# Optimization experiments

Measured on AMD Instinct MI355X. Metric: run time of the kernel, lower is better.

## Reference

```python
import jax, jax.numpy as jnp
import numpy as np

B, S, D = 4, 1024, 1024   # batch, seq_len, d_model (isize=hsize=osize)
H, AD = 16, 64            # num_head, attn_dim = hsize // num_head
K_REL = 16                # k_rel_pos (bidirectional: 2*K+1 = 33 embeddings)
EPS = 1e-8                # SparseNormer eps (ieps_default)


def setup_inputs() -> dict:
    key = jax.random.key(0)
    ks = jax.random.split(key, 5)
    scale = 0.02
    return {
        "iQ": jax.random.normal(ks[0], (B, S, D), jnp.float32),
        "Wa": jax.random.normal(ks[1], (3 * D, D), jnp.float32) * scale,   # adaptor weight
        "ba": jnp.zeros((3 * D,), jnp.float32),                            # adaptor bias
        "rel_emb": jax.random.normal(ks[2], (2 * K_REL + 1, AD), jnp.float32) * scale,
        "sn_bias": jnp.zeros((1,), jnp.float32),                           # SparseNormer bias
        "Wo": jax.random.normal(ks[3], (D, D), jnp.float32) * scale,       # outer weight
        "bo": jnp.zeros((D,), jnp.float32),                                # outer bias
    }


def reference(iQ, Wa, ba, rel_emb, sn_bias, Wo, bo):
    b, s, _ = iQ.shape
    # fused QKV projection: [B,S,3*H*AD] -> q,k,v each [B,H,S,AD]
    qkv = (iQ @ Wa.T + ba).reshape(b, s, 3, H, AD)
    q = qkv[:, :, 0].transpose(0, 2, 1, 3)
    k = qkv[:, :, 1].transpose(0, 2, 1, 3)
    v = qkv[:, :, 2].transpose(0, 2, 1, 3)

    # content scores [B,H,S,S]
    scores = jnp.einsum('bhqd,bhkd->bhqk', q, k)

    # relative-position term: rel_pos[i,j] = clip(j-i, -K, K) + K
    pos = jnp.arange(s)
    rp = jnp.clip(pos[None, :] - pos[:, None], -K_REL, K_REL) + K_REL  # [S,S] int
    r = rel_emb[rp]                                                     # [S,S,AD]
    scores = scores + jnp.einsum('bhqd,qkd->bhqk', q, r)

    scores = scores / jnp.sqrt(jnp.asarray(AD, scores.dtype))

    # SparseNormer: relu(x + b)^2 / (sum + eps)
    t = jax.nn.relu(scores + sn_bias)
    t = t * t
    attn = t / (t.sum(-1, keepdims=True) + EPS)

    ctx = jnp.einsum('bhqk,bhkd->bhqd', attn, v)          # [B,H,S,AD]
    ctx = ctx.transpose(0, 2, 1, 3).reshape(b, s, H * AD)  # [B,S,hsize]
    return ctx @ Wo.T + bo
```

## Files before the change

### kernel.cpp

```cpp
#include <hip/hip_runtime.h>
#include <hip/hip_bf16.h>
#include <stdint.h>

typedef unsigned short u16;
typedef unsigned int   u32;
typedef __attribute__((ext_vector_type(8))) __bf16 bf16x8;
typedef __attribute__((ext_vector_type(4))) float  f32x4;
typedef __attribute__((ext_vector_type(2))) u32    u32x2;

#define B_  4
#define S_  1024
#define D_  1024
#define H_  16
#define AD_ 64

#if defined(__has_builtin)
#if __has_builtin(__builtin_amdgcn_cvt_pk_bf16_f32)
#define HAVE_CVT_PK 1
#endif
#if __has_builtin(__builtin_amdgcn_global_load_lds)
#define HAVE_GLL 1
#endif
#endif

#ifdef HAVE_CVT_PK
typedef __attribute__((ext_vector_type(2))) __bf16 bf16x2;
__device__ __forceinline__ u32 pack2(float a, float b) {
    bf16x2 r = __builtin_amdgcn_cvt_pk_bf16_f32(a, b);
    return __builtin_bit_cast(u32, r);
}
__device__ __forceinline__ u16 f2bf(float f) {
    return (u16)pack2(f, f);
}
#else
__device__ __forceinline__ u16 f2bf(float f) {
    u32 u = __float_as_uint(f);
    u32 r = u + 0x7fffu + ((u >> 16) & 1u);
    return (u16)(r >> 16);
}
__device__ __forceinline__ u32 pack2(float a, float b) {
    return (u32)f2bf(a) | ((u32)f2bf(b) << 16);
}
#endif

typedef __attribute__((address_space(1))) const u32 gas_u32;
typedef __attribute__((address_space(3))) u32 las_u32;
__device__ __forceinline__ void gll16(const void* g, void* l) {
#ifdef HAVE_GLL
    __builtin_amdgcn_global_load_lds((gas_u32*)g, (las_u32*)l, 16, 0, 0);
#else
    int lane = threadIdx.x & 63;
    *(uint4*)((u16*)l + lane * 8) = *(const uint4*)g;
#endif
}

__global__ __launch_bounds__(256) void conv_bf16(
    const float* __restrict__ a, const float* __restrict__ b,
    const float* __restrict__ c,
    u16* __restrict__ ao, u16* __restrict__ bo, u16* __restrict__ co,
    int na, int nb)
{
    int gid = blockIdx.x * 256 + threadIdx.x;
    int base = gid * 8;
    const float* src; u16* dst; int off;
    if (base < na)           { src = a; dst = ao; off = base; }
    else if (base < na + nb) { src = b; dst = bo; off = base - na; }
    else                     { src = c; dst = co; off = base - na - nb; }
    float4 v0 = *(const float4*)(src + off);
    float4 v1 = *(const float4*)(src + off + 4);
    u32 pk[4] = {pack2(v0.x, v0.y), pack2(v0.z, v0.w),
                 pack2(v1.x, v1.y), pack2(v1.z, v1.w)};
    *(uint4*)(dst + off) = *(uint4*)pk;
}

__global__ __launch_bounds__(256) void qkv_gemm(
    const u16* __restrict__ A, const u16* __restrict__ W,
    const float* __restrict__ bias,
    u16* __restrict__ qb, u16* __restrict__ kb, u16* __restrict__ vb)
{
    __shared__ u16 As[128 * 64];
    __shared__ u16 Bs[128 * 64];

    const int tid  = threadIdx.x;
    const int lane = tid & 63, w = tid >> 6;
    const int quad = lane >> 4, ln = lane & 15;
    const int wrow = (w >> 1) * 64, wcol = (w & 1) * 64;
    const int row0 = blockIdx.y * 128, col0 = blockIdx.x * 128;

    const int ri = lane >> 3, ci = lane & 7;
    const int scol = (ci ^ ri) << 3;

    f32x4 acc[4][4];
#pragma unroll
    for (int i = 0; i < 4; i++)
#pragma unroll
        for (int j = 0; j < 4; j++) acc[i][j] = (f32x4){0.f, 0.f, 0.f, 0.f};

    for (int kb_i = 0; kb_i < 16; ++kb_i) {
        const int k0 = kb_i * 64;
#pragma unroll
        for (int c = 0; c < 4; ++c) {
            int r0 = c * 32 + w * 8;
            int gr = r0 + ri;
            gll16(A + (size_t)(row0 + gr) * D_ + k0 + scol, &As[r0 * 64]);
            gll16(W + (size_t)(col0 + gr) * D_ + k0 + scol, &Bs[r0 * 64]);
        }
        __syncthreads();
#pragma unroll
        for (int ks = 0; ks < 2; ++ks) {
            bf16x8 af[4], bfr[4];
#pragma unroll
            for (int mt = 0; mt < 4; ++mt) {
                int r = wrow + mt * 16 + ln;
                af[mt] = *(bf16x8*)&As[r * 64 + (((ks * 4 + quad) ^ (r & 7)) << 3)];
            }
#pragma unroll
            for (int nt = 0; nt < 4; ++nt) {
                int r = wcol + nt * 16 + ln;
                bfr[nt] = *(bf16x8*)&Bs[r * 64 + (((ks * 4 + quad) ^ (r & 7)) << 3)];
            }
#pragma unroll
            for (int mt = 0; mt < 4; ++mt)
#pragma unroll
                for (int nt = 0; nt < 4; ++nt)
                    acc[mt][nt] = __builtin_amdgcn_mfma_f32_16x16x32_bf16(
                        af[mt], bfr[nt], acc[mt][nt], 0, 0, 0);
        }
        __syncthreads();
    }

    const int which = col0 >> 10;
#pragma unroll
    for (int mt = 0; mt < 4; ++mt) {
#pragma unroll
        for (int nt = 0; nt < 4; ++nt) {
            int n = col0 + wcol + nt * 16 + ln;
            float bv = bias[n];
            int h = (n >> 6) & 15, d = n & 63;
            if (which == 2) {
                int m0 = row0 + wrow + mt * 16 + quad * 4;
                int b = m0 >> 10, s0 = m0 & 1023;
                u32x2 pk;
                pk.x = pack2(acc[mt][nt][0] + bv, acc[mt][nt][1] + bv);
                pk.y = pack2(acc[mt][nt][2] + bv, acc[mt][nt][3] + bv);
                *(u32x2*)&vb[((size_t)((b * 16 + h) * 64 + d)) * 1024 + s0] = pk;
            } else {
#pragma unroll
                for (int reg = 0; reg < 4; ++reg) {
                    int m = row0 + wrow + mt * 16 + quad * 4 + reg;
                    int b = m >> 10, s = m & 1023;
                    float v = acc[mt][nt][reg] + bv;
                    if (which == 0)
                        qb[((size_t)((b * 16 + h) * 1024 + s)) * 64 + d] = f2bf(v * 0.125f);
                    else
                        kb[((size_t)((b * 16 + h) * 1024 + s)) * 64 + d] = f2bf(v);
                }
            }
        }
    }
}

__global__ __launch_bounds__(256) void attn_kernel(
    const u16* __restrict__ qb, const u16* __restrict__ kb,
    const u16* __restrict__ vb, const float* __restrict__ rel,
    const float* __restrict__ snb_p, u16* __restrict__ ctx)
{
    __shared__ u16 q_s[64 * 64];
    __shared__ u16 k_s[64 * 64];
    __shared__ u16 v_s[64 * 64];
    __shared__ u16 t_s[64 * 64];
    __shared__ float qr[33 * 64];

    u16* rel_s = t_s;

    const int tid  = threadIdx.x;
    const int lane = tid & 63, w = tid >> 6;
    const int quad = lane >> 4, ln = lane & 15;
    const int strip = w * 16;
    const int bh = blockIdx.x >> 4, qt = blockIdx.x & 15;
    const int i0 = qt * 64;
    const float snb = snb_p[0];

    const u16* qplane = qb + ((size_t)bh * 1024 + i0) * 64;
    const u16* kplane = kb + (size_t)bh * 1024 * 64;
    const u16* vplane = vb + (size_t)bh * 64 * 1024;

    const int ri = lane >> 3, ci = lane & 7;
    const int scol = (ci ^ ri) << 3;

#pragma unroll
    for (int c = 0; c < 2; ++c) {
        int r0 = w * 16 + c * 8;
        int gr = r0 + ri;
        gll16(qplane + (size_t)gr * 64 + scol, &q_s[r0 * 64]);
    }
    for (int idx = tid; idx < 384; idx += 256) {
        int p = idx >> 3, c = idx & 7;
        u32 pk[4];
        if (p < 33) {
            const float* sp = rel + p * 64 + c * 8;
            float4 r0 = *(const float4*)sp;
            float4 r1 = *(const float4*)(sp + 4);
            pk[0] = pack2(r0.x, r0.y); pk[1] = pack2(r0.z, r0.w);
            pk[2] = pack2(r1.x, r1.y); pk[3] = pack2(r1.z, r1.w);
        } else { pk[0] = pk[1] = pk[2] = pk[3] = 0; }
        *(uint4*)&rel_s[p * 64 + ((c ^ (p & 7)) << 3)] = *(uint4*)pk;
    }
    __syncthreads();

    {
        f32x4 qacc[3];
#pragma unroll
        for (int nt = 0; nt < 3; ++nt) qacc[nt] = (f32x4){0.f, 0.f, 0.f, 0.f};
#pragma unroll
        for (int ks = 0; ks < 2; ++ks) {
            int rq = strip + ln;
            bf16x8 aq = *(bf16x8*)&q_s[rq * 64 + (((ks * 4 + quad) ^ (rq & 7)) << 3)];
#pragma unroll
            for (int nt = 0; nt < 3; ++nt) {
                int rp = nt * 16 + ln;
                bf16x8 bp = *(bf16x8*)&rel_s[rp * 64 + (((ks * 4 + quad) ^ (rp & 7)) << 3)];
                qacc[nt] = __builtin_amdgcn_mfma_f32_16x16x32_bf16(aq, bp, qacc[nt], 0, 0, 0);
            }
        }
#pragma unroll
        for (int nt = 0; nt < 3; ++nt) {
            int p = nt * 16 + ln;
            if (p < 33) {
#pragma unroll
                for (int reg = 0; reg < 4; ++reg)
                    qr[p * 64 + strip + quad * 4 + reg] = qacc[nt][reg];
            }
        }
    }
    __syncthreads();

    const int iloc = strip + ln;
    const float cL = qr[iloc] + snb;
    const float cR = qr[32 * 64 + iloc] + snb;

    bf16x8 bq[2];
#pragma unroll
    for (int ks = 0; ks < 2; ++ks)
        bq[ks] = *(bf16x8*)&q_s[iloc * 64 + (((ks * 4 + quad) ^ (iloc & 7)) << 3)];

    float Lsum = 0.f;
    f32x4 o_acc[4];
#pragma unroll
    for (int nt = 0; nt < 4; ++nt) o_acc[nt] = (f32x4){0.f, 0.f, 0.f, 0.f};

    for (int jt = 0; jt < 16; ++jt) {
        const int j0 = jt * 64;
        __syncthreads();
#pragma unroll
        for (int c = 0; c < 2; ++c) {
            int r0 = w * 16 + c * 8;
            int gr = r0 + ri;
            gll16(kplane + (size_t)(j0 + gr) * 64 + scol, &k_s[r0 * 64]);
            gll16(vplane + (size_t)gr * 1024 + j0 + scol, &v_s[r0 * 64]);
        }
        __syncthreads();

        f32x4 sacc[4];
#pragma unroll
        for (int mj = 0; mj < 4; ++mj) sacc[mj] = (f32x4){0.f, 0.f, 0.f, 0.f};
#pragma unroll
        for (int ks = 0; ks < 2; ++ks) {
#pragma unroll
            for (int mj = 0; mj < 4; ++mj) {
                int rk = mj * 16 + ln;
                bf16x8 ak = *(bf16x8*)&k_s[rk * 64 + (((ks * 4 + quad) ^ (rk & 7)) << 3)];
                sacc[mj] = __builtin_amdgcn_mfma_f32_16x16x32_bf16(ak, bq[ks], sacc[mj], 0, 0, 0);
            }
        }

        const int d0 = j0 - i0;
        if (d0 <= -128 || d0 >= 128) {
            const float c = (d0 < 0) ? cL : cR;
#pragma unroll
            for (int mj = 0; mj < 4; ++mj) {
                float tv[4];
#pragma unroll
                for (int reg = 0; reg < 4; ++reg) {
                    float t = fmaxf(sacc[mj][reg] + c, 0.f);
                    t = t * t;
                    Lsum += t;
                    tv[reg] = t;
                }
                u32x2 pk;
                pk.x = pack2(tv[0], tv[1]);
                pk.y = pack2(tv[2], tv[3]);
                int jl = mj * 16 + quad * 4;
                int chunk = (jl >> 3) ^ (iloc & 7);
                *(u32x2*)&t_s[iloc * 64 + (chunk << 3) + (quad & 1) * 4] = pk;
            }
        } else {
#pragma unroll
            for (int mj = 0; mj < 4; ++mj) {
                int jbase = j0 + mj * 16 + quad * 4;
                float tv[4];
#pragma unroll
                for (int reg = 0; reg < 4; ++reg) {
                    int dlt = jbase + reg - (i0 + iloc);
                    int p = min(max(dlt, -16), 16) + 16;
                    float t = fmaxf(sacc[mj][reg] + qr[p * 64 + iloc] + snb, 0.f);
                    t = t * t;
                    Lsum += t;
                    tv[reg] = t;
                }
                u32x2 pk;
                pk.x = pack2(tv[0], tv[1]);
                pk.y = pack2(tv[2], tv[3]);
                int jl = mj * 16 + quad * 4;
                int chunk = (jl >> 3) ^ (iloc & 7);
                *(u32x2*)&t_s[iloc * 64 + (chunk << 3) + (quad & 1) * 4] = pk;
            }
        }

#pragma unroll
        for (int ks = 0; ks < 2; ++ks) {
            bf16x8 at = *(bf16x8*)&t_s[iloc * 64 + (((ks * 4 + quad) ^ (iloc & 7)) << 3)];
#pragma unroll
            for (int nt = 0; nt < 4; ++nt) {
                int rv = nt * 16 + ln;
                bf16x8 bv = *(bf16x8*)&v_s[rv * 64 + (((ks * 4 + quad) ^ (rv & 7)) << 3)];
                o_acc[nt] = __builtin_amdgcn_mfma_f32_16x16x32_bf16(at, bv, o_acc[nt], 0, 0, 0);
            }
        }
    }

    Lsum += __shfl_xor(Lsum, 16);
    Lsum += __shfl_xor(Lsum, 32);
    float Linv = 1.f / (Lsum + 1e-8f);

    const int b = bh >> 4, h = bh & 15;
#pragma unroll
    for (int reg = 0; reg < 4; ++reg) {
        int ig = i0 + strip + quad * 4 + reg;
        float li = __shfl(Linv, quad * 4 + reg);
#pragma unroll
        for (int nt = 0; nt < 4; ++nt) {
            int dg = nt * 16 + ln;
            ctx[((size_t)(b * 1024 + ig)) * 1024 + h * 64 + dg] =
                f2bf(o_acc[nt][reg] * li);
        }
    }
}

__global__ __launch_bounds__(256) void out_gemm(
    const u16* __restrict__ A, const u16* __restrict__ W,
    const float* __restrict__ bias, float* __restrict__ out)
{
    __shared__ u16 As[128 * 64];
    __shared__ u16 Bs[128 * 64];

    const int tid  = threadIdx.x;
    const int lane = tid & 63, w = tid >> 6;
    const int quad = lane >> 4, ln = lane & 15;
    const int wrow = (w >> 1) * 64, wcol = (w & 1) * 64;
    const int row0 = blockIdx.y * 128, col0 = blockIdx.x * 128;

    const int ri = lane >> 3, ci = lane & 7;
    const int scol = (ci ^ ri) << 3;

    f32x4 acc[4][4];
#pragma unroll
    for (int i = 0; i < 4; i++)
#pragma unroll
        for (int j = 0; j < 4; j++) acc[i][j] = (f32x4){0.f, 0.f, 0.f, 0.f};

    for (int kb_i = 0; kb_i < 16; ++kb_i) {
        const int k0 = kb_i * 64;
#pragma unroll
        for (int c = 0; c < 4; ++c) {
            int r0 = c * 32 + w * 8;
            int gr = r0 + ri;
            gll16(A + (size_t)(row0 + gr) * D_ + k0 + scol, &As[r0 * 64]);
            gll16(W + (size_t)(col0 + gr) * D_ + k0 + scol, &Bs[r0 * 64]);
        }
        __syncthreads();
#pragma unroll
        for (int ks = 0; ks < 2; ++ks) {
            bf16x8 af[4], bfr[4];
#pragma unroll
            for (int mt = 0; mt < 4; ++mt) {
                int r = wrow + mt * 16 + ln;
                af[mt] = *(bf16x8*)&As[r * 64 + (((ks * 4 + quad) ^ (r & 7)) << 3)];
            }
#pragma unroll
            for (int nt = 0; nt < 4; ++nt) {
                int r = wcol + nt * 16 + ln;
                bfr[nt] = *(bf16x8*)&Bs[r * 64 + (((ks * 4 + quad) ^ (r & 7)) << 3)];
            }
#pragma unroll
            for (int mt = 0; mt < 4; ++mt)
#pragma unroll
                for (int nt = 0; nt < 4; ++nt)
                    acc[mt][nt] = __builtin_amdgcn_mfma_f32_16x16x32_bf16(
                        af[mt], bfr[nt], acc[mt][nt], 0, 0, 0);
        }
        __syncthreads();
    }
#pragma unroll
    for (int mt = 0; mt < 4; ++mt) {
#pragma unroll
        for (int nt = 0; nt < 4; ++nt) {
            int n = col0 + wcol + nt * 16 + ln;
            float bv = bias[n];
#pragma unroll
            for (int reg = 0; reg < 4; ++reg) {
                int m = row0 + wrow + mt * 16 + quad * 4 + reg;
                out[(size_t)m * D_ + n] = acc[mt][nt][reg] + bv;
            }
        }
    }
}

extern "C" void kernel_launch(void* const* d_in, const int* in_sizes, int n_in,
                              void* d_out, int out_size, void* d_ws, size_t ws_size,
                              hipStream_t stream)
{
    const float* iQ  = (const float*)d_in[0];
    const float* Wa  = (const float*)d_in[1];
    const float* ba  = (const float*)d_in[2];
    const float* rel = (const float*)d_in[3];
    const float* snb = (const float*)d_in[4];
    const float* Wo  = (const float*)d_in[5];
    const float* bo  = (const float*)d_in[6];
    float* out = (float*)d_out;

    const size_t NQ = (size_t)B_ * S_ * D_;
    const size_t NWA = (size_t)3 * D_ * D_;
    const size_t NWO = (size_t)D_ * D_;
    const size_t PLANE = (size_t)B_ * H_ * S_ * AD_;

    u16* iQbf = (u16*)d_ws;
    u16* Wabf = iQbf + NQ;
    u16* Wobf = Wabf + NWA;
    u16* qbuf = Wobf + NWO;
    u16* kbuf = qbuf + PLANE;
    u16* vbuf = kbuf + PLANE;
    u16* ctx  = iQbf;

    conv_bf16<<<4096, 256, 0, stream>>>(iQ, Wa, Wo, iQbf, Wabf, Wobf,
                                        (int)NQ, (int)NWA);
    qkv_gemm<<<dim3(24, 32), 256, 0, stream>>>(iQbf, Wabf, ba, qbuf, kbuf, vbuf);
    attn_kernel<<<dim3(1024), 256, 0, stream>>>(qbuf, kbuf, vbuf, rel, snb, ctx);
    out_gemm<<<dim3(8, 32), 256, 0, stream>>>(ctx, Wobf, bo, out);
}
```

Before: 196.7 us.

## Fuse all stages into one persistent cooperative kernel with grid syncs

Replaces the four separate launches (bf16 conversion, QKV GEMM, attention, output GEMM) with a single persistent cooperative kernel. Blocks loop over tiles and separate the stages with grid-wide syncs, which removes launch gaps and inter-kernel drains. The attention stage also double-buffers the K/V tiles so the next tile is prefetched during compute, and the output GEMM uses 128x64 tiles so more blocks can share the work. The costs are grid.sync overhead, a grid capped by occupancy that may leave some stages underfilled, and a fallback to the multi-kernel path if the cooperative launch fails.

```diff
diff --git a/kernel.cpp b/kernel.cpp
--- a/kernel.cpp
+++ b/kernel.cpp
@@ -1,6 +1,9 @@
 #include <hip/hip_runtime.h>
+#include <hip/hip_cooperative_groups.h>
 #include <hip/hip_bf16.h>
 #include <stdint.h>
+
+namespace cg = cooperative_groups;
 
 typedef unsigned short u16;
 typedef unsigned int   u32;
@@ -29,9 +32,7 @@
     bf16x2 r = __builtin_amdgcn_cvt_pk_bf16_f32(a, b);
     return __builtin_bit_cast(u32, r);
 }
-__device__ __forceinline__ u16 f2bf(float f) {
-    return (u16)pack2(f, f);
-}
+__device__ __forceinline__ u16 f2bf(float f) { return (u16)pack2(f, f); }
 #else
 __device__ __forceinline__ u16 f2bf(float f) {
     u32 u = __float_as_uint(f);
@@ -52,6 +53,374 @@
     int lane = threadIdx.x & 63;
     *(uint4*)((u16*)l + lane * 8) = *(const uint4*)g;
 #endif
+}
+
+#define SMEM_BYTES 49408
+
+__global__ void __launch_bounds__(256, 3) fused_pipeline(
+    const float* __restrict__ iQ, const float* __restrict__ Wa,
+    const float* __restrict__ ba, const float* __restrict__ rel,
+    const float* __restrict__ snb_p, const float* __restrict__ Wo,
+    const float* __restrict__ bo, float* __restrict__ out,
+    u16* iQbf, u16* Wabf, u16* Wobf, u16* qbuf, u16* kbuf, u16* vbuf)
+{
+    __shared__ __align__(16) char smem[SMEM_BYTES];
+    cg::grid_group grid = cg::this_grid();
+    const int nblk = gridDim.x;
+
+    const int tid  = threadIdx.x;
+    const int lane = tid & 63, w = tid >> 6;
+    const int quad = lane >> 4, ln = lane & 15;
+    const int ri = lane >> 3, ci = lane & 7;
+    const int scol = (ci ^ ri) << 3;
+
+    {
+        const int NQ = B_ * S_ * D_;
+        const int NWA = 3 * D_ * D_;
+        const int NT = NQ + NWA + D_ * D_;
+        const int stride = nblk * 256 * 8;
+        for (int base = (blockIdx.x * 256 + tid) * 8; base < NT; base += stride) {
+            const float* src; u16* dst; int off;
+            if (base < NQ)            { src = iQ; dst = iQbf; off = base; }
+            else if (base < NQ + NWA) { src = Wa; dst = Wabf; off = base - NQ; }
+            else                      { src = Wo; dst = Wobf; off = base - NQ - NWA; }
+            float4 v0 = *(const float4*)(src + off);
+            float4 v1 = *(const float4*)(src + off + 4);
+            u32 pk[4] = {pack2(v0.x, v0.y), pack2(v0.z, v0.w),
+                         pack2(v1.x, v1.y), pack2(v1.z, v1.w)};
+            *(uint4*)(dst + off) = *(uint4*)pk;
+        }
+    }
+    __threadfence();
+    grid.sync();
+
+    {
+        u16* As = (u16*)smem;
+        u16* Bs = (u16*)(smem + 16384);
+        const int wrow = (w >> 1) * 64, wcol = (w & 1) * 64;
+
+        for (int t = blockIdx.x; t < 768; t += nblk) {
+            const int row0 = (t / 24) * 128, col0 = (t % 24) * 128;
+
+            f32x4 acc[4][4];
+#pragma unroll
+            for (int i = 0; i < 4; i++)
+#pragma unroll
+                for (int j = 0; j < 4; j++) acc[i][j] = (f32x4){0.f, 0.f, 0.f, 0.f};
+
+            for (int kb_i = 0; kb_i < 16; ++kb_i) {
+                const int k0 = kb_i * 64;
+#pragma unroll
+                for (int c = 0; c < 4; ++c) {
+                    int r0 = c * 32 + w * 8;
+                    int gr = r0 + ri;
+                    gll16(iQbf + (size_t)(row0 + gr) * D_ + k0 + scol, &As[r0 * 64]);
+                    gll16(Wabf + (size_t)(col0 + gr) * D_ + k0 + scol, &Bs[r0 * 64]);
+                }
+                __syncthreads();
+#pragma unroll
+                for (int ks = 0; ks < 2; ++ks) {
+                    bf16x8 af[4], bfr[4];
+#pragma unroll
+                    for (int mt = 0; mt < 4; ++mt) {
+                        int r = wrow + mt * 16 + ln;
+                        af[mt] = *(bf16x8*)&As[r * 64 + (((ks * 4 + quad) ^ (r & 7)) << 3)];
+                    }
+#pragma unroll
+                    for (int nt = 0; nt < 4; ++nt) {
+                        int r = wcol + nt * 16 + ln;
+                        bfr[nt] = *(bf16x8*)&Bs[r * 64 + (((ks * 4 + quad) ^ (r & 7)) << 3)];
+                    }
+#pragma unroll
+                    for (int mt = 0; mt < 4; ++mt)
+#pragma unroll
+                        for (int nt = 0; nt < 4; ++nt)
+                            acc[mt][nt] = __builtin_amdgcn_mfma_f32_16x16x32_bf16(
+                                af[mt], bfr[nt], acc[mt][nt], 0, 0, 0);
+                }
+                __syncthreads();
+            }
+
+            const int which = col0 >> 10;
+#pragma unroll
+            for (int mt = 0; mt < 4; ++mt) {
+#pragma unroll
+                for (int nt = 0; nt < 4; ++nt) {
+                    int n = col0 + wcol + nt * 16 + ln;
+                    float bv = ba[n];
+                    int h = (n >> 6) & 15, d = n & 63;
+                    if (which == 2) {
+                        int m0 = row0 + wrow + mt * 16 + quad * 4;
+                        int b = m0 >> 10, s0 = m0 & 1023;
+                        u32x2 pk;
+                        pk.x = pack2(acc[mt][nt][0] + bv, acc[mt][nt][1] + bv);
+                        pk.y = pack2(acc[mt][nt][2] + bv, acc[mt][nt][3] + bv);
+                        *(u32x2*)&vbuf[((size_t)((b * 16 + h) * 64 + d)) * 1024 + s0] = pk;
+                    } else {
+#pragma unroll
+                        for (int reg = 0; reg < 4; ++reg) {
+                            int m = row0 + wrow + mt * 16 + quad * 4 + reg;
+                            int b = m >> 10, s = m & 1023;
+                            float v = acc[mt][nt][reg] + bv;
+                            if (which == 0)
+                                qbuf[((size_t)((b * 16 + h) * 1024 + s)) * 64 + d] = f2bf(v * 0.125f);
+                            else
+                                kbuf[((size_t)((b * 16 + h) * 1024 + s)) * 64 + d] = f2bf(v);
+                        }
+                    }
+                }
+            }
+        }
+    }
+    __threadfence();
+    grid.sync();
+
+    {
+        u16* q_s = (u16*)smem;
+        u16* k0b = (u16*)(smem + 8192);
+        u16* k1b = (u16*)(smem + 16384);
+        u16* v0b = (u16*)(smem + 24576);
+        u16* v1b = (u16*)(smem + 32768);
+        float* qr = (float*)(smem + 40960);
+        u16* t_s = q_s;
+        u16* rel_s = v1b;
+
+        u16* ctx = iQbf;
+        const float snb = snb_p[0];
+        const int strip = w * 16;
+
+        for (int t = blockIdx.x; t < 1024; t += nblk) {
+            const int bh = t >> 4, qt = t & 15;
+            const int i0 = qt * 64;
+            const u16* qplane = qbuf + ((size_t)bh * 1024 + i0) * 64;
+            const u16* kplane = kbuf + (size_t)bh * 1024 * 64;
+            const u16* vplane = vbuf + (size_t)bh * 64 * 1024;
+
+#pragma unroll
+            for (int c = 0; c < 2; ++c) {
+                int r0 = strip + c * 8;
+                gll16(qplane + (size_t)(r0 + ri) * 64 + scol, &q_s[r0 * 64]);
+            }
+            for (int idx = tid; idx < 384; idx += 256) {
+                int p = idx >> 3, c = idx & 7;
+                u32 pk[4];
+                if (p < 33) {
+                    const float* sp = rel + p * 64 + c * 8;
+                    float4 r0 = *(const float4*)sp;
+                    float4 r1 = *(const float4*)(sp + 4);
+                    pk[0] = pack2(r0.x, r0.y); pk[1] = pack2(r0.z, r0.w);
+                    pk[2] = pack2(r1.x, r1.y); pk[3] = pack2(r1.z, r1.w);
+                } else { pk[0] = pk[1] = pk[2] = pk[3] = 0; }
+                *(uint4*)&rel_s[p * 64 + ((c ^ (p & 7)) << 3)] = *(uint4*)pk;
+            }
+            __syncthreads();
+
+            const int iloc = strip + ln;
+            bf16x8 bq[2];
+#pragma unroll
+            for (int ks = 0; ks < 2; ++ks)
+                bq[ks] = *(bf16x8*)&q_s[iloc * 64 + (((ks * 4 + quad) ^ (iloc & 7)) << 3)];
+
+            {
+                f32x4 qacc[3];
+#pragma unroll
+                for (int nt = 0; nt < 3; ++nt) qacc[nt] = (f32x4){0.f, 0.f, 0.f, 0.f};
+#pragma unroll
+                for (int ks = 0; ks < 2; ++ks) {
+#pragma unroll
+                    for (int nt = 0; nt < 3; ++nt) {
+                        int rp = nt * 16 + ln;
+                        bf16x8 bp = *(bf16x8*)&rel_s[rp * 64 + (((ks * 4 + quad) ^ (rp & 7)) << 3)];
+                        qacc[nt] = __builtin_amdgcn_mfma_f32_16x16x32_bf16(bq[ks], bp, qacc[nt], 0, 0, 0);
+                    }
+                }
+#pragma unroll
+                for (int nt = 0; nt < 3; ++nt) {
+                    int p = nt * 16 + ln;
+                    if (p < 33) {
+#pragma unroll
+                        for (int reg = 0; reg < 4; ++reg)
+                            qr[p * 64 + strip + quad * 4 + reg] = qacc[nt][reg];
+                    }
+                }
+            }
+#pragma unroll
+            for (int c = 0; c < 2; ++c) {
+                int r0 = strip + c * 8;
+                gll16(kplane + (size_t)(r0 + ri) * 64 + scol, &k0b[r0 * 64]);
+                gll16(vplane + (size_t)(r0 + ri) * 1024 + scol, &v0b[r0 * 64]);
+            }
+            __syncthreads();
+
+            const float cL = qr[iloc] + snb;
+            const float cR = qr[32 * 64 + iloc] + snb;
+
+            float Lsum = 0.f;
+            f32x4 o_acc[4];
+#pragma unroll
+            for (int nt = 0; nt < 4; ++nt) o_acc[nt] = (f32x4){0.f, 0.f, 0.f, 0.f};
+
+            for (int jt = 0; jt < 16; ++jt) {
+                const int j0 = jt * 64;
+                u16* kc = (jt & 1) ? k1b : k0b;
+                u16* vc = (jt & 1) ? v1b : v0b;
+                if (jt < 15) {
+                    u16* kn = (jt & 1) ? k0b : k1b;
+                    u16* vn = (jt & 1) ? v0b : v1b;
+#pragma unroll
+                    for (int c = 0; c < 2; ++c) {
+                        int r0 = strip + c * 8;
+                        gll16(kplane + (size_t)(j0 + 64 + r0 + ri) * 64 + scol, &kn[r0 * 64]);
+                        gll16(vplane + (size_t)(r0 + ri) * 1024 + (j0 + 64) + scol, &vn[r0 * 64]);
+                    }
+                }
+
+                f32x4 sacc[4];
+#pragma unroll
+                for (int mj = 0; mj < 4; ++mj) sacc[mj] = (f32x4){0.f, 0.f, 0.f, 0.f};
+#pragma unroll
+                for (int ks = 0; ks < 2; ++ks) {
+#pragma unroll
+                    for (int mj = 0; mj < 4; ++mj) {
+                        int rk = mj * 16 + ln;
+                        bf16x8 ak = *(bf16x8*)&kc[rk * 64 + (((ks * 4 + quad) ^ (rk & 7)) << 3)];
+                        sacc[mj] = __builtin_amdgcn_mfma_f32_16x16x32_bf16(ak, bq[ks], sacc[mj], 0, 0, 0);
+                    }
+                }
+
+                const int ib = i0 + strip;
+#pragma unroll
+                for (int mj = 0; mj < 4; ++mj) {
+                    const int jg0 = j0 + mj * 16;
+                    const int diff = jg0 - ib;
+                    float tv[4];
+                    if (diff >= 32 || diff <= -32) {
+                        const float c = (diff < 0) ? cL : cR;
+#pragma unroll
+                        for (int reg = 0; reg < 4; ++reg) {
+                            float tt = fmaxf(sacc[mj][reg] + c, 0.f);
+                            tt = tt * tt;
+                            Lsum += tt;
+                            tv[reg] = tt;
+                        }
+                    } else {
+#pragma unroll
+                        for (int reg = 0; reg < 4; ++reg) {
+                            int dlt = jg0 + quad * 4 + reg - (ib + ln);
+                            int p = min(max(dlt, -16), 16) + 16;
+                            float tt = fmaxf(sacc[mj][reg] + qr[p * 64 + iloc] + snb, 0.f);
+                            tt = tt * tt;
+                            Lsum += tt;
+                            tv[reg] = tt;
+                        }
+                    }
+                    u32x2 pk;
+                    pk.x = pack2(tv[0], tv[1]);
+                    pk.y = pack2(tv[2], tv[3]);
+                    int chunk = (2 * mj + (quad >> 1)) ^ (iloc & 7);
+                    *(u32x2*)&t_s[iloc * 64 + (chunk << 3) + (quad & 1) * 4] = pk;
+                }
+
+#pragma unroll
+                for (int ks = 0; ks < 2; ++ks) {
+                    bf16x8 at = *(bf16x8*)&t_s[iloc * 64 + (((ks * 4 + quad) ^ (iloc & 7)) << 3)];
+#pragma unroll
+                    for (int nt = 0; nt < 4; ++nt) {
+                        int rv = nt * 16 + ln;
+                        bf16x8 bv = *(bf16x8*)&vc[rv * 64 + (((ks * 4 + quad) ^ (rv & 7)) << 3)];
+                        o_acc[nt] = __builtin_amdgcn_mfma_f32_16x16x32_bf16(at, bv, o_acc[nt], 0, 0, 0);
+                    }
+                }
+                __syncthreads();
+            }
+
+            Lsum += __shfl_xor(Lsum, 16);
+            Lsum += __shfl_xor(Lsum, 32);
+            float Linv = 1.f / (Lsum + 1e-8f);
+
+            const int b = bh >> 4, h = bh & 15;
+#pragma unroll
+            for (int reg = 0; reg < 4; ++reg) {
+                int ig = i0 + strip + quad * 4 + reg;
+                float li = __shfl(Linv, quad * 4 + reg);
+#pragma unroll
+                for (int nt = 0; nt < 4; ++nt) {
+                    int dg = nt * 16 + ln;
+                    ctx[((size_t)(b * 1024 + ig)) * 1024 + h * 64 + dg] =
+                        f2bf(o_acc[nt][reg] * li);
+                }
+            }
+            __syncthreads();
+        }
+    }
+    __threadfence();
+    grid.sync();
+
+    {
+        u16* As = (u16*)smem;
+        u16* Bs = (u16*)(smem + 16384);
+        const u16* ctx = iQbf;
+        const int wrow = (w >> 1) * 64, wcol = (w & 1) * 32;
+
+        for (int t = blockIdx.x; t < 512; t += nblk) {
+            const int row0 = (t >> 4) * 128, col0 = (t & 15) * 64;
+
+            f32x4 acc[4][2];
+#pragma unroll
+            for (int i = 0; i < 4; i++)
+#pragma unroll
+                for (int j = 0; j < 2; j++) acc[i][j] = (f32x4){0.f, 0.f, 0.f, 0.f};
+
+            for (int kb_i = 0; kb_i < 16; ++kb_i) {
+                const int k0 = kb_i * 64;
+#pragma unroll
+                for (int c = 0; c < 4; ++c) {
+                    int r0 = c * 32 + w * 8;
+                    gll16(ctx + (size_t)(row0 + r0 + ri) * D_ + k0 + scol, &As[r0 * 64]);
+                }
+#pragma unroll
+                for (int c = 0; c < 2; ++c) {
+                    int r0 = c * 32 + w * 8;
+                    gll16(Wobf + (size_t)(col0 + r0 + ri) * D_ + k0 + scol, &Bs[r0 * 64]);
+                }
+                __syncthreads();
+#pragma unroll
+                for (int ks = 0; ks < 2; ++ks) {
+                    bf16x8 af[4], bfr[2];
+#pragma unroll
+                    for (int mt = 0; mt < 4; ++mt) {
+                        int r = wrow + mt * 16 + ln;
+                        af[mt] = *(bf16x8*)&As[r * 64 + (((ks * 4 + quad) ^ (r & 7)) << 3)];
+                    }
+#pragma unroll
+                    for (int nt = 0; nt < 2; ++nt) {
+                        int r = wcol + nt * 16 + ln;
+                        bfr[nt] = *(bf16x8*)&Bs[r * 64 + (((ks * 4 + quad) ^ (r & 7)) << 3)];
+                    }
+#pragma unroll
+                    for (int mt = 0; mt < 4; ++mt)
+#pragma unroll
+                        for (int nt = 0; nt < 2; ++nt)
+                            acc[mt][nt] = __builtin_amdgcn_mfma_f32_16x16x32_bf16(
+                                af[mt], bfr[nt], acc[mt][nt], 0, 0, 0);
+                }
+                __syncthreads();
+            }
+#pragma unroll
+            for (int mt = 0; mt < 4; ++mt) {
+#pragma unroll
+                for (int nt = 0; nt < 2; ++nt) {
+                    int n = col0 + wcol + nt * 16 + ln;
+                    float bv = bo[n];
+#pragma unroll
+                    for (int reg = 0; reg < 4; ++reg) {
+                        int m = row0 + wrow + mt * 16 + quad * 4 + reg;
+                        out[(size_t)m * D_ + n] = acc[mt][nt][reg] + bv;
+                    }
+                }
+            }
+        }
+    }
 }
 
 __global__ __launch_bounds__(256) void conv_bf16(
@@ -80,13 +449,11 @@
 {
     __shared__ u16 As[128 * 64];
     __shared__ u16 Bs[128 * 64];
-
     const int tid  = threadIdx.x;
     const int lane = tid & 63, w = tid >> 6;
     const int quad = lane >> 4, ln = lane & 15;
     const int wrow = (w >> 1) * 64, wcol = (w & 1) * 64;
     const int row0 = blockIdx.y * 128, col0 = blockIdx.x * 128;
-
     const int ri = lane >> 3, ci = lane & 7;
     const int scol = (ci ^ ri) << 3;
 
@@ -128,7 +495,6 @@
         }
         __syncthreads();
     }
-
     const int which = col0 >> 10;
 #pragma unroll
     for (int mt = 0; mt < 4; ++mt) {
@@ -166,12 +532,11 @@
     const float* __restrict__ snb_p, u16* __restrict__ ctx)
 {
     __shared__ u16 q_s[64 * 64];
-    __shared__ u16 k_s[64 * 64];
-    __shared__ u16 v_s[64 * 64];
-    __shared__ u16 t_s[64 * 64];
+    __shared__ u16 k_s[2][64 * 64];
+    __shared__ u16 v_s[2][64 * 64];
     __shared__ float qr[33 * 64];
-
-    u16* rel_s = t_s;
+    u16* t_s = q_s;
+    u16* rel_s = v_s[1];
 
     const int tid  = threadIdx.x;
     const int lane = tid & 63, w = tid >> 6;
@@ -184,15 +549,13 @@
     const u16* qplane = qb + ((size_t)bh * 1024 + i0) * 64;
     const u16* kplane = kb + (size_t)bh * 1024 * 64;
     const u16* vplane = vb + (size_t)bh * 64 * 1024;
-
     const int ri = lane >> 3, ci = lane & 7;
     const int scol = (ci ^ ri) << 3;
 
 #pragma unroll
     for (int c = 0; c < 2; ++c) {
-        int r0 = w * 16 + c * 8;
-        int gr = r0 + ri;
-        gll16(qplane + (size_t)gr * 64 + scol, &q_s[r0 * 64]);
+        int r0 = strip + c * 8;
+        gll16(qplane + (size_t)(r0 + ri) * 64 + scol, &q_s[r0 * 64]);
     }
     for (int idx = tid; idx < 384; idx += 256) {
         int p = idx >> 3, c = idx & 7;
@@ -208,19 +571,23 @@
     }
     __syncthreads();
 
+    const int iloc = strip + ln;
+    bf16x8 bq[2];
+#pragma unroll
+    for (int ks = 0; ks < 2; ++ks)
+        bq[ks] = *(bf16x8*)&q_s[iloc * 64 + (((ks * 4 + quad) ^ (iloc & 7)) << 3)];
+
     {
         f32x4 qacc[3];
 #pragma unroll
         for (int nt = 0; nt < 3; ++nt) qacc[nt] = (f32x4){0.f, 0.f, 0.f, 0.f};
 #pragma unroll
         for (int ks = 0; ks < 2; ++ks) {
-            int rq = strip + ln;
-            bf16x8 aq = *(bf16x8*)&q_s[rq * 64 + (((ks * 4 + quad) ^ (rq & 7)) << 3)];
 #pragma unroll
             for (int nt = 0; nt < 3; ++nt) {
                 int rp = nt * 16 + ln;
                 bf16x8 bp = *(bf16x8*)&rel_s[rp * 64 + (((ks * 4 + quad) ^ (rp & 7)) << 3)];
-                qacc[nt] = __builtin_amdgcn_mfma_f32_16x16x32_bf16(aq, bp, qacc[nt], 0, 0, 0);
+                qacc[nt] = __builtin_amdgcn_mfma_f32_16x16x32_bf16(bq[ks], bp, qacc[nt], 0, 0, 0);
             }
         }
 #pragma unroll
@@ -233,17 +600,17 @@
             }
         }
     }
+#pragma unroll
+    for (int c = 0; c < 2; ++c) {
+        int r0 = strip + c * 8;
+        gll16(kplane + (size_t)(r0 + ri) * 64 + scol, &k_s[0][r0 * 64]);
+        gll16(vplane + (size_t)(r0 + ri) * 1024 + scol, &v_s[0][r0 * 64]);
+    }
     __syncthreads();
 
-    const int iloc = strip + ln;
     const float cL = qr[iloc] + snb;
     const float cR = qr[32 * 64 + iloc] + snb;
 
-    bf16x8 bq[2];
-#pragma unroll
-    for (int ks = 0; ks < 2; ++ks)
-        bq[ks] = *(bf16x8*)&q_s[iloc * 64 + (((ks * 4 + quad) ^ (iloc & 7)) << 3)];
-
     float Lsum = 0.f;
     f32x4 o_acc[4];
 #pragma unroll
@@ -251,16 +618,18 @@
 
     for (int jt = 0; jt < 16; ++jt) {
         const int j0 = jt * 64;
-        __syncthreads();
-#pragma unroll
-        for (int c = 0; c < 2; ++c) {
-            int r0 = w * 16 + c * 8;
-            int gr = r0 + ri;
-            gll16(kplane + (size_t)(j0 + gr) * 64 + scol, &k_s[r0 * 64]);
-            gll16(vplane + (size_t)gr * 1024 + j0 + scol, &v_s[r0 * 64]);
-        }
-        __syncthreads();
-
+        u16* kc = k_s[jt & 1];
+        u16* vc = v_s[jt & 1];
+        if (jt < 15) {
+            u16* kn = k_s[1 - (jt & 1)];
+            u16* vn = v_s[1 - (jt & 1)];
+#pragma unroll
+            for (int c = 0; c < 2; ++c) {
+                int r0 = strip + c * 8;
+                gll16(kplane + (size_t)(j0 + 64 + r0 + ri) * 64 + scol, &kn[r0 * 64]);
+                gll16(vplane + (size_t)(r0 + ri) * 1024 + (j0 + 64) + scol, &vn[r0 * 64]);
+            }
+        }
         f32x4 sacc[4];
 #pragma unroll
         for (int mj = 0; mj < 4; ++mj) sacc[mj] = (f32x4){0.f, 0.f, 0.f, 0.f};
@@ -269,70 +638,58 @@
 #pragma unroll
             for (int mj = 0; mj < 4; ++mj) {
                 int rk = mj * 16 + ln;
-                bf16x8 ak = *(bf16x8*)&k_s[rk * 64 + (((ks * 4 + quad) ^ (rk & 7)) << 3)];
+                bf16x8 ak = *(bf16x8*)&kc[rk * 64 + (((ks * 4 + quad) ^ (rk & 7)) << 3)];
                 sacc[mj] = __builtin_amdgcn_mfma_f32_16x16x32_bf16(ak, bq[ks], sacc[mj], 0, 0, 0);
             }
         }
-
-        const int d0 = j0 - i0;
-        if (d0 <= -128 || d0 >= 128) {
-            const float c = (d0 < 0) ? cL : cR;
-#pragma unroll
-            for (int mj = 0; mj < 4; ++mj) {
-                float tv[4];
+        const int ib = i0 + strip;
+#pragma unroll
+        for (int mj = 0; mj < 4; ++mj) {
+            const int jg0 = j0 + mj * 16;
+            const int diff = jg0 - ib;
+            float tv[4];
+            if (diff >= 32 || diff <= -32) {
+                const float c = (diff < 0) ? cL : cR;
 #pragma unroll
                 for (int reg = 0; reg < 4; ++reg) {
-                    float t = fmaxf(sacc[mj][reg] + c, 0.f);
-                    t = t * t;
-                    Lsum += t;
-                    tv[reg] = t;
-                }
-                u32x2 pk;
-                pk.x = pack2(tv[0], tv[1]);
-                pk.y = pack2(tv[2], tv[3]);
-                int jl = mj * 16 + quad * 4;
-                int chunk = (jl >> 3) ^ (iloc & 7);
-                *(u32x2*)&t_s[iloc * 64 + (chunk << 3) + (quad & 1) * 4] = pk;
-            }
-        } else {
-#pragma unroll
-            for (int mj = 0; mj < 4; ++mj) {
-                int jbase = j0 + mj * 16 + quad * 4;
-                float tv[4];
+                    float tt = fmaxf(sacc[mj][reg] + c, 0.f);
+                    tt = tt * tt;
+                    Lsum += tt;
+                    tv[reg] = tt;
+                }
+            } else {
 #pragma unroll
                 for (int reg = 0; reg < 4; ++reg) {
-                    int dlt = jbase + reg - (i0 + iloc);
+                    int dlt = jg0 + quad * 4 + reg - (ib + ln);
                     int p = min(max(dlt, -16), 16) + 16;
-                    float t = fmaxf(sacc[mj][reg] + qr[p * 64 + iloc] + snb, 0.f);
-                    t = t * t;
-                    Lsum += t;
-                    tv[reg] = t;
-                }
-                u32x2 pk;
-                pk.x = pack2(tv[0], tv[1]);
-                pk.y = pack2(tv[2], tv[3]);
-                int jl = mj * 16 + quad * 4;
-                int chunk = (jl >> 3) ^ (iloc & 7);
-                *(u32x2*)&t_s[iloc * 64 + (chunk << 3) + (quad & 1) * 4] = pk;
-            }
-        }
-
+                    float tt = fmaxf(sacc[mj][reg] + qr[p * 64 + iloc] + snb, 0.f);
+                    tt = tt * tt;
+                    Lsum += tt;
+                    tv[reg] = tt;
+                }
+            }
+            u32x2 pk;
+            pk.x = pack2(tv[0], tv[1]);
+            pk.y = pack2(tv[2], tv[3]);
+            int chunk = (2 * mj + (quad >> 1)) ^ (iloc & 7);
+            *(u32x2*)&t_s[iloc * 64 + (chunk << 3) + (quad & 1) * 4] = pk;
+        }
 #pragma unroll
         for (int ks = 0; ks < 2; ++ks) {
             bf16x8 at = *(bf16x8*)&t_s[iloc * 64 + (((ks * 4 + quad) ^ (iloc & 7)) << 3)];
 #pragma unroll
             for (int nt = 0; nt < 4; ++nt) {
                 int rv = nt * 16 + ln;
-                bf16x8 bv = *(bf16x8*)&v_s[rv * 64 + (((ks * 4 + quad) ^ (rv & 7)) << 3)];
+                bf16x8 bv = *(bf16x8*)&vc[rv * 64 + (((ks * 4 + quad) ^ (rv & 7)) << 3)];
                 o_acc[nt] = __builtin_amdgcn_mfma_f32_16x16x32_bf16(at, bv, o_acc[nt], 0, 0, 0);
             }
         }
+        __syncthreads();
     }
 
     Lsum += __shfl_xor(Lsum, 16);
     Lsum += __shfl_xor(Lsum, 32);
     float Linv = 1.f / (Lsum + 1e-8f);
-
     const int b = bh >> 4, h = bh & 15;
 #pragma unroll
     for (int reg = 0; reg < 4; ++reg) {
@@ -352,50 +709,51 @@
     const float* __restrict__ bias, float* __restrict__ out)
 {
     __shared__ u16 As[128 * 64];
-    __shared__ u16 Bs[128 * 64];
-
+    __shared__ u16 Bs[64 * 64];
     const int tid  = threadIdx.x;
     const int lane = tid & 63, w = tid >> 6;
     const int quad = lane >> 4, ln = lane & 15;
-    const int wrow = (w >> 1) * 64, wcol = (w & 1) * 64;
-    const int row0 = blockIdx.y * 128, col0 = blockIdx.x * 128;
-
+    const int wrow = (w >> 1) * 64, wcol = (w & 1) * 32;
+    const int row0 = blockIdx.y * 128, col0 = blockIdx.x * 64;
     const int ri = lane >> 3, ci = lane & 7;
     const int scol = (ci ^ ri) << 3;
 
-    f32x4 acc[4][4];
+    f32x4 acc[4][2];
 #pragma unroll
     for (int i = 0; i < 4; i++)
 #pragma unroll
-        for (int j = 0; j < 4; j++) acc[i][j] = (f32x4){0.f, 0.f, 0.f, 0.f};
+        for (int j = 0; j < 2; j++) acc[i][j] = (f32x4){0.f, 0.f, 0.f, 0.f};
 
     for (int kb_i = 0; kb_i < 16; ++kb_i) {
         const int k0 = kb_i * 64;
 #pragma unroll
         for (int c = 0; c < 4; ++c) {
             int r0 = c * 32 + w * 8;
-            int gr = r0 + ri;
-            gll16(A + (size_t)(row0 + gr) * D_ + k0 + scol, &As[r0 * 64]);
-            gll16(W + (size_t)(col0 + gr) * D_ + k0 + scol, &Bs[r0 * 64]);
+            gll16(A + (size_t)(row0 + r0 + ri) * D_ + k0 + scol, &As[r0 * 64]);
+        }
+#pragma unroll
+        for (int c = 0; c < 2; ++c) {
+            int r0 = c * 32 + w * 8;
+            gll16(W + (size_t)(col0 + r0 + ri) * D_ + k0 + scol, &Bs[r0 * 64]);
         }
         __syncthreads();
 #pragma unroll
         for (int ks = 0; ks < 2; ++ks) {
-            bf16x8 af[4], bfr[4];
+            bf16x8 af[4], bfr[2];
 #pragma unroll
             for (int mt = 0; mt < 4; ++mt) {
                 int r = wrow + mt * 16 + ln;
                 af[mt] = *(bf16x8*)&As[r * 64 + (((ks * 4 + quad) ^ (r & 7)) << 3)];
             }
 #pragma unroll
-            for (int nt = 0; nt < 4; ++nt) {
+            for (int nt = 0; nt < 2; ++nt) {
                 int r = wcol + nt * 16 + ln;
                 bfr[nt] = *(bf16x8*)&Bs[r * 64 + (((ks * 4 + quad) ^ (r & 7)) << 3)];
             }
 #pragma unroll
             for (int mt = 0; mt < 4; ++mt)
 #pragma unroll
-                for (int nt = 0; nt < 4; ++nt)
+                for (int nt = 0; nt < 2; ++nt)
                     acc[mt][nt] = __builtin_amdgcn_mfma_f32_16x16x32_bf16(
                         af[mt], bfr[nt], acc[mt][nt], 0, 0, 0);
         }
@@ -404,7 +762,7 @@
 #pragma unroll
     for (int mt = 0; mt < 4; ++mt) {
 #pragma unroll
-        for (int nt = 0; nt < 4; ++nt) {
+        for (int nt = 0; nt < 2; ++nt) {
             int n = col0 + wcol + nt * 16 + ln;
             float bv = bias[n];
 #pragma unroll
@@ -427,7 +785,7 @@
     const float* snb = (const float*)d_in[4];
     const float* Wo  = (const float*)d_in[5];
     const float* bo  = (const float*)d_in[6];
-    float* out = (float*)d_out;
+    float* outp = (float*)d_out;
 
     const size_t NQ = (size_t)B_ * S_ * D_;
     const size_t NWA = (size_t)3 * D_ * D_;
@@ -440,11 +798,33 @@
     u16* qbuf = Wobf + NWO;
     u16* kbuf = qbuf + PLANE;
     u16* vbuf = kbuf + PLANE;
-    u16* ctx  = iQbf;
-
-    conv_bf16<<<4096, 256, 0, stream>>>(iQ, Wa, Wo, iQbf, Wabf, Wobf,
-                                        (int)NQ, (int)NWA);
-    qkv_gemm<<<dim3(24, 32), 256, 0, stream>>>(iQbf, Wabf, ba, qbuf, kbuf, vbuf);
-    attn_kernel<<<dim3(1024), 256, 0, stream>>>(qbuf, kbuf, vbuf, rel, snb, ctx);
-    out_gemm<<<dim3(8, 32), 256, 0, stream>>>(ctx, Wobf, bo, out);
-}
+
+    int maxPerCU = 0;
+    hipError_t qerr = hipOccupancyMaxActiveBlocksPerMultiprocessor(
+        &maxPerCU, (const void*)fused_pipeline, 256, 0);
+    int grid = 0;
+    if (qerr == hipSuccess && maxPerCU > 0) {
+        grid = maxPerCU * 256;
+        if (grid > 768) grid = 768;
+    }
+
+    hipError_t lerr = hipErrorUnknown;
+    if (grid > 0) {
+        void* args[] = {
+            (void*)&iQ, (void*)&Wa, (void*)&ba, (void*)&rel, (void*)&snb,
+            (void*)&Wo, (void*)&bo, (void*)&outp,
+            (void*)&iQbf, (void*)&Wabf, (void*)&Wobf,
+            (void*)&qbuf, (void*)&kbuf, (void*)&vbuf,
+        };
+        lerr = hipLaunchCooperativeKernel((void*)fused_pipeline, dim3(grid),
+                                          dim3(256), args, 0, stream);
+    }
+    if (lerr != hipSuccess) {
+        (void)hipGetLastError();
+        conv_bf16<<<4096, 256, 0, stream>>>(iQ, Wa, Wo, iQbf, Wabf, Wobf,
+                                            (int)NQ, (int)NWA);
+        qkv_gemm<<<dim3(24, 32), 256, 0, stream>>>(iQbf, Wabf, ba, qbuf, kbuf, vbuf);
+        attn_kernel<<<dim3(1024), 256, 0, stream>>>(qbuf, kbuf, vbuf, rel, snb, iQbf);
+        out_gemm<<<dim3(16, 32), 256, 0, stream>>>(iQbf, Wobf, bo, outp);
+    }
+}
```

Measured after the change: 435.2 us. 121% more time.
